# Performance work log

Hardware: AMD Instinct MI355X
Metric: run time of the kernel (lower is better)

Reference implementation:

```python
import jax, jax.numpy as jnp
import numpy as np

B, D, C, W, H = 2, 8, 256, 84, 84
NUM_HEADS = 8
WS = (2, 7, 7)
SS = (1, 3, 3)
MLP_RATIO = 4
EPS = 1e-5


def _rel_pos_index(ws):
    # static int index table (N, N), matches WindowAttention3D buffer
    coords = np.stack(np.meshgrid(np.arange(ws[0]), np.arange(ws[1]), np.arange(ws[2]), indexing='ij'))
    cf = coords.reshape(3, -1)
    rel = (cf[:, :, None] - cf[:, None, :]).transpose(1, 2, 0).copy()
    rel[:, :, 0] += ws[0] - 1
    rel[:, :, 1] += ws[1] - 1
    rel[:, :, 2] += ws[2] - 1
    rel[:, :, 0] *= (2 * ws[1] - 1) * (2 * ws[2] - 1)
    rel[:, :, 1] *= 2 * ws[2] - 1
    return rel.sum(-1)


def _attn_mask(Dp, Hp, Wp, ws, ss):
    # static additive shift mask (nW, N, N), matches create_mask
    m = np.zeros((Dp, Hp, Wp))
    cnt = 0
    for d in (slice(0, -ws[0]), slice(-ws[0], -ss[0]), slice(-ss[0], None)):
        for h in (slice(0, -ws[1]), slice(-ws[1], -ss[1]), slice(-ss[1], None)):
            for w in (slice(0, -ws[2]), slice(-ws[2], -ss[2]), slice(-ss[2], None)):
                m[d, h, w] = cnt
                cnt += 1
    mw = m.reshape(Dp // ws[0], ws[0], Hp // ws[1], ws[1], Wp // ws[2], ws[2])
    mw = mw.transpose(0, 2, 4, 1, 3, 5).reshape(-1, ws[0] * ws[1] * ws[2])
    diff = mw[:, None, :] - mw[:, :, None]
    return np.where(diff != 0, -100.0, 0.0).astype(np.float32)


def _layernorm(x, g, b):
    mu = x.mean(-1, keepdims=True)
    var = ((x - mu) ** 2).mean(-1, keepdims=True)
    return (x - mu) * jax.lax.rsqrt(var + EPS) * g + b


def setup_inputs():
    key = jax.random.key(0)
    ks = jax.random.split(key, 6)
    hidden = C * MLP_RATIO
    nbias = (2 * WS[0] - 1) * (2 * WS[1] - 1) * (2 * WS[2] - 1)
    s = lambda k, shape, sc=0.02: jax.random.normal(k, shape, jnp.float32) * sc
    return dict(
        x=jax.random.normal(ks[0], (B, D, C, W, H), jnp.float32),
        norm1_g=jnp.ones((C,), jnp.float32), norm1_b=jnp.zeros((C,), jnp.float32),
        qkv_w=s(ks[1], (3 * C, C)),
        rpb_table=s(ks[2], (nbias, NUM_HEADS)),
        proj_w=s(ks[3], (C, C)), proj_b=jnp.zeros((C,), jnp.float32),
        norm2_g=jnp.ones((C,), jnp.float32), norm2_b=jnp.zeros((C,), jnp.float32),
        fc1_w=s(ks[4], (hidden, C)), fc1_b=jnp.zeros((hidden,), jnp.float32),
        fc2_w=s(ks[5], (C, hidden)), fc2_b=jnp.zeros((C,), jnp.float32),
    )


def reference(x, norm1_g, norm1_b, qkv_w, rpb_table, proj_w, proj_b,
              norm2_g, norm2_b, fc1_w, fc1_b, fc2_w, fc2_b):
    # x: (B, D, C, W, H) -> (B, D, H, W, C)
    xp = jnp.transpose(x, (0, 1, 4, 3, 2))
    Bn, Dn, Hn, Wn, Cn = xp.shape
    wd, wh, ww = WS
    N = wd * wh * ww
    nW = (Dn // wd) * (Hn // wh) * (Wn // ww)
    head_dim = Cn // NUM_HEADS
    scale = head_dim ** -0.5

    rel_idx = _rel_pos_index(WS)                      # (N, N) static
    mask = jnp.asarray(_attn_mask(Dn, Hn, Wn, WS, SS))  # (nW, N, N) static

    shortcut = xp
    h1 = _layernorm(xp, norm1_g, norm1_b)
    # cyclic shift (D,H,W divisible by window -> no padding)
    h1 = jnp.roll(h1, shift=(-SS[0], -SS[1], -SS[2]), axis=(1, 2, 3))
    # window partition -> (B*nW, N, C)
    xw = h1.reshape(Bn, Dn // wd, wd, Hn // wh, wh, Wn // ww, ww, Cn)
    xw = jnp.transpose(xw, (0, 1, 3, 5, 2, 4, 6, 7)).reshape(-1, N, Cn)
    B_ = xw.shape[0]

    qkv = (xw @ qkv_w.T).reshape(B_, N, 3, NUM_HEADS, head_dim)
    qkv = jnp.transpose(qkv, (2, 0, 3, 1, 4))  # (3, B_, h, N, hd)
    q, k, v = qkv[0] * scale, qkv[1], qkv[2]
    attn = jnp.einsum('bhnd,bhmd->bhnm', q, k)
    bias = rpb_table[rel_idx.reshape(-1)].reshape(N, N, NUM_HEADS)
    attn = attn + jnp.transpose(bias, (2, 0, 1))[None]
    attn = attn.reshape(Bn, nW, NUM_HEADS, N, N) + mask[None, :, None]
    attn = jax.nn.softmax(attn.reshape(B_, NUM_HEADS, N, N), axis=-1)
    out = jnp.einsum('bhnm,bhmd->bhnd', attn, v)
    out = jnp.transpose(out, (0, 2, 1, 3)).reshape(B_, N, Cn)
    out = out @ proj_w.T + proj_b

    # window reverse -> (B, D, H, W, C)
    out = out.reshape(Bn, Dn // wd, Hn // wh, Wn // ww, wd, wh, ww, Cn)
    out = jnp.transpose(out, (0, 1, 4, 2, 5, 3, 6, 7)).reshape(Bn, Dn, Hn, Wn, Cn)
    out = jnp.roll(out, shift=(SS[0], SS[1], SS[2]), axis=(1, 2, 3))

    xres = shortcut + out
    # MLP block (torch GELU = exact erf)
    h2 = _layernorm(xres, norm2_g, norm2_b)
    h2 = jax.nn.gelu(h2 @ fc1_w.T + fc1_b, approximate=False)
    h2 = h2 @ fc2_w.T + fc2_b
    y = xres + h2
    return jnp.transpose(y, (0, 1, 4, 3, 2))  # back to (B, D, C, W, H)
```

## Files before the change

kernel.cpp:

```cpp
#include <hip/hip_runtime.h>
#include <hip/hip_bf16.h>
#include <cstdint>
#include <cstddef>

#define B_   2
#define D_   8
#define C_   256
#define W_   84
#define H_   84
#define NH   8
#define HD   32
#define NTOK 98
#define WH   7056
#define M2   56448
#define NWC  576

typedef __attribute__((ext_vector_type(8))) short sh8;
typedef __attribute__((ext_vector_type(4))) float f32x4;
typedef __hip_bfloat16 bf16;

__global__ __launch_bounds__(256) void k_f2b(const float* __restrict__ in,
                                             bf16* __restrict__ out, int n) {
  int i = blockIdx.x * 256 + threadIdx.x;
  if (i < n) out[i] = __float2bfloat16(in[i]);
}

__global__ __launch_bounds__(256) void k_bias(const float* __restrict__ rpb,
                                              float* __restrict__ tbl) {
  int cls = blockIdx.x >> 3, h = blockIdx.x & 7;
  int dB = cls >> 2, hB = (cls >> 1) & 1, wB = cls & 1;
  for (int idx = threadIdx.x; idx < 112 * 112; idx += 256) {
    int r = idx / 112, c = idx - (idx / 112) * 112;
    int rt = r < 98 ? r : 97, ct = c < 98 ? c : 97;
    int jdr = rt / 49, remr = rt % 49, jhr = remr / 7, jwr = remr % 7;
    int jdc = ct / 49, remc = ct % 49, jhc = remc / 7, jwc = remc % 7;
    int bir = jdr * 169 + jhr * 13 + jwr, bic = jdc * 169 + jhc * 13 + jwc;
    int dgr = dB ? ((6 + jdr) < 7 ? 1 : 2) : 0;
    int hgr = hB ? ((77 + jhr) < 81 ? 1 : 2) : 0;
    int wgr = wB ? ((77 + jwr) < 81 ? 1 : 2) : 0;
    int dgc = dB ? ((6 + jdc) < 7 ? 1 : 2) : 0;
    int hgc = hB ? ((77 + jhc) < 81 ? 1 : 2) : 0;
    int wgc = wB ? ((77 + jwc) < 81 ? 1 : 2) : 0;
    int cir = dgr * 9 + hgr * 3 + wgr, cic = dgc * 9 + hgc * 3 + wgc;
    float v = rpb[(bir - bic + 253) * 8 + h] + (cir == cic ? 0.f : -100.f);
    tbl[((size_t)(cls * 8 + h) * 112 + r) * 112 + c] = v;
  }
}

__device__ __forceinline__ int inv_row(int b, int d0, int w0, int h0) {
  int sd = (d0 + 7) & 7;
  int lid = (sd >> 1) & 1, jd = sd & 1;
  int sh = h0 + 81; if (sh >= 84) sh -= 84;
  int sw = w0 + 81; if (sw >= 84) sw -= 84;
  int ih = sh / 7, jh = sh - ih * 7;
  int iw = sw / 7, jw = sw - iw * 7;
  return (b * 288 + lid * 144 + ih * 12 + iw) * 98 + jd * 49 + jh * 7 + jw;
}

__global__ __launch_bounds__(256) void k_xpose_w(const float* __restrict__ x,
                                                 float* __restrict__ xtw, int cchunk) {
  int blk = blockIdx.x;
  int ch = blk & 1;
  int t = blk >> 1;
  int w0 = t % 84;
  int t2 = t / 84;
  int i = t2 & 3, b = t2 >> 2;
  int d0 = (cchunk * 4 + 1 + i) & 7;
  __shared__ float tile[128][85];
  __shared__ int rtab[84];
  int tid = threadIdx.x;
  if (tid < 84) rtab[tid] = inv_row(b, d0, w0, tid);
  const float* src = x + ((size_t)(b * 8 + d0) * 256 + ch * 128) * WH + w0 * 84;
  for (int idx = tid; idx < 128 * 21; idx += 256) {
    int c = idx / 21, h4 = idx - c * 21;
    float4 v = *(const float4*)(src + (size_t)c * WH + h4 * 4);
    tile[c][h4 * 4 + 0] = v.x; tile[c][h4 * 4 + 1] = v.y;
    tile[c][h4 * 4 + 2] = v.z; tile[c][h4 * 4 + 3] = v.w;
  }
  __syncthreads();
  for (int idx = tid; idx < 84 * 128; idx += 256) {
    int h = idx >> 7, cc = idx & 127;
    xtw[(size_t)rtab[h] * 256 + ch * 128 + cc] = tile[cc][h];
  }
}

__global__ __launch_bounds__(256) void k_ln1_lin(
    const float* __restrict__ xtw, const float* __restrict__ g,
    const float* __restrict__ bb, bf16* __restrict__ xw) {
  int rl = blockIdx.x * 4 + (threadIdx.x >> 6);
  int lane = threadIdx.x & 63;
  int c0 = lane * 4;
  float4 v = *(const float4*)(xtw + (size_t)rl * 256 + c0);
  float s = v.x + v.y + v.z + v.w;
  float s2 = v.x * v.x + v.y * v.y + v.z * v.z + v.w * v.w;
#pragma unroll
  for (int off = 32; off; off >>= 1) { s += __shfl_xor(s, off, 64); s2 += __shfl_xor(s2, off, 64); }
  float mu = s * (1.f / 256.f);
  float var = s2 * (1.f / 256.f) - mu * mu;
  float rs = rsqrtf(var + 1e-5f);
  float4 gg = *(const float4*)(g + c0);
  float4 bv = *(const float4*)(bb + c0);
  bf16 tmp[4];
  tmp[0] = __float2bfloat16((v.x - mu) * rs * gg.x + bv.x);
  tmp[1] = __float2bfloat16((v.y - mu) * rs * gg.y + bv.y);
  tmp[2] = __float2bfloat16((v.z - mu) * rs * gg.z + bv.z);
  tmp[3] = __float2bfloat16((v.w - mu) * rs * gg.w + bv.w);
  *(ushort4*)(&xw[(size_t)rl * 256 + c0]) = *(ushort4*)tmp;
}

__device__ __forceinline__ float gelu_fast(float v) {
  float x = v * 0.70710678118f;
  float ax = fabsf(x);
  float t = 1.0f / (1.0f + 0.3275911f * ax);
  float y = t * (0.254829592f + t * (-0.284496736f +
            t * (1.421413741f + t * (-1.453152027f + t * 1.061405429f))));
  float er = 1.0f - y * __expf(-ax * ax);
  er = copysignf(er, x);
  return 0.5f * v * (1.0f + er);
}

template <int EPI>
__global__ __launch_bounds__(256) void k_gemm_bt(
    const bf16* __restrict__ A, const bf16* __restrict__ Bw,
    int M, int N, int K,
    const float* __restrict__ bias, const float* __restrict__ res,
    void* __restrict__ outv) {
  __shared__ __align__(16) short smem[24576];
  int nwg = gridDim.x;
  int orig = blockIdx.x;
  int q8 = nwg >> 3, r8 = nwg & 7;
  int xcd = orig & 7, lwg = orig >> 3;
  int bid = (xcd < r8 ? xcd * (q8 + 1) : r8 * (q8 + 1) + (xcd - r8) * q8) + lwg;
  int nbn = N >> 7;
  int bm = bid / nbn, bn = bid - bm * nbn;
  int tid = threadIdx.x;
  int lane = tid & 63, wv = tid >> 6;
  int wr = wv >> 1, wc = wv & 1;
  f32x4 acc[4][4] = {};
  const short* Ag = (const short*)A + (size_t)bm * 128 * K;
  const short* Bg = (const short*)Bw + (size_t)bn * 128 * K;
  int rIn = lane >> 2;
  int cSrc = ((lane & 3) ^ ((lane >> 3) & 3)) * 8;
  int nk = K >> 5;

  auto stage = [&](int buf, int kt) {
    short* sA = smem + buf * 8192;
    short* sB = sA + 4096;
#pragma unroll
    for (int rr = 0; rr < 2; ++rr) {
      int r0 = wv * 32 + rr * 16;
      const short* ga = Ag + (size_t)(r0 + rIn) * K + kt * 32 + cSrc;
      const short* gb = Bg + (size_t)(r0 + rIn) * K + kt * 32 + cSrc;
      __builtin_amdgcn_global_load_lds(
          (const __attribute__((address_space(1))) void*)ga,
          (__attribute__((address_space(3))) void*)&sA[r0 * 32], 16, 0, 0);
      __builtin_amdgcn_global_load_lds(
          (const __attribute__((address_space(1))) void*)gb,
          (__attribute__((address_space(3))) void*)&sB[r0 * 32], 16, 0, 0);
    }
  };

  stage(0, 0);
  stage(1, 1);
  int rdBuf = 0, wrBuf = 2;
  int rb = wr * 64 + (lane & 15);
  int cb = wc * 64 + (lane & 15);
  int kswz = (((lane >> 4) ^ ((lane >> 1) & 3))) * 8;
  for (int kt = 0; kt < nk; ++kt) {
    __builtin_amdgcn_s_barrier();
    if (kt + 2 < nk) {
      stage(wrBuf, kt + 2);
      asm volatile("s_waitcnt vmcnt(8)" ::: "memory");
    } else if (kt + 1 < nk) {
      asm volatile("s_waitcnt vmcnt(4)" ::: "memory");
    } else {
      asm volatile("s_waitcnt vmcnt(0)" ::: "memory");
    }
    __builtin_amdgcn_s_barrier();
    __builtin_amdgcn_sched_barrier(0);
    const short* sA = smem + rdBuf * 8192;
    const short* sB = sA + 4096;
    sh8 af[4], bfr[4];
#pragma unroll
    for (int m = 0; m < 4; ++m) af[m] = *(const sh8*)&sA[(rb + m * 16) * 32 + kswz];
#pragma unroll
    for (int n2 = 0; n2 < 4; ++n2) bfr[n2] = *(const sh8*)&sB[(cb + n2 * 16) * 32 + kswz];
#pragma unroll
    for (int m = 0; m < 4; ++m)
#pragma unroll
      for (int n2 = 0; n2 < 4; ++n2)
        acc[m][n2] = __builtin_amdgcn_mfma_f32_16x16x32_bf16(af[m], bfr[n2], acc[m][n2], 0, 0, 0);
    rdBuf = (rdBuf + 1 == 3) ? 0 : rdBuf + 1;
    wrBuf = (wrBuf + 1 == 3) ? 0 : wrBuf + 1;
  }
  int rbase = bm * 128 + wr * 64 + ((lane >> 4) << 2);
  int cbase = bn * 128 + wc * 64 + (lane & 15);
#pragma unroll
  for (int m = 0; m < 4; ++m) {
#pragma unroll
    for (int j = 0; j < 4; ++j) {
      int r = rbase + m * 16 + j;
#pragma unroll
      for (int n2 = 0; n2 < 4; ++n2) {
        int cc = cbase + n2 * 16;
        float v = acc[m][n2][j];
        if (EPI == 2) {
          v += bias[cc] + res[(size_t)r * N + cc];
          ((float*)outv)[(size_t)r * N + cc] = v;
        } else {
          if (bias) v += bias[cc];
          if (EPI == 1) v = gelu_fast(v);
          ((bf16*)outv)[(size_t)r * N + cc] = __float2bfloat16(v);
        }
      }
    }
  }
}

__global__ __launch_bounds__(64) void k_attn_mfma(
    const bf16* __restrict__ qkv, const float* __restrict__ tbl,
    bf16* __restrict__ aout, int idbase) {
  int blk = blockIdx.x;
  int wl = blk >> 3, h = blk & 7;
  int lid = (wl / 144) & 1;
  int id = idbase + lid;
  int rem = wl % 144;
  int ih = rem / 12, iw = rem - ih * 12;
  int cls = ((id == 3) ? 4 : 0) + ((ih == 11) ? 2 : 0) + ((iw == 11) ? 1 : 0);
  const float* bt = tbl + (size_t)(cls * 8 + h) * 112 * 112;
  int lane = threadIdx.x;
  __shared__ __align__(16) short vt[32][136];
  __shared__ __align__(16) short pb[16][136];
  sh8 z = {};
  for (int i = lane; i < 544; i += 64) *((sh8*)&vt[0][0] + i) = z;
  for (int i = lane; i < 272; i += 64) *((sh8*)&pb[0][0] + i) = z;
  __syncthreads();
  const size_t base = (size_t)wl * NTOK * 768;
  for (int i = lane; i < 98 * 8; i += 64) {
    int c = i >> 3, d4 = (i & 7) * 4;
    ushort4 vu = *(const ushort4*)&qkv[base + (size_t)c * 768 + 512 + h * 32 + d4];
    vt[d4 + 0][c] = (short)vu.x; vt[d4 + 1][c] = (short)vu.y;
    vt[d4 + 2][c] = (short)vu.z; vt[d4 + 3][c] = (short)vu.w;
  }
  int kq = (lane >> 4) * 8;
  sh8 kf[7];
#pragma unroll
  for (int jt = 0; jt < 7; ++jt) {
    int c = jt * 16 + (lane & 15);
    kf[jt] = *(const sh8*)&qkv[base + (size_t)c * 768 + 256 + h * 32 + kq];
  }
  __syncthreads();
  sh8 vb[2][4];
#pragma unroll
  for (int dt = 0; dt < 2; ++dt)
#pragma unroll
    for (int k2 = 0; k2 < 4; ++k2)
      vb[dt][k2] = *(const sh8*)&vt[dt * 16 + (lane & 15)][k2 * 32 + kq];

  const float scale = 0.17677669529663687f;
  f32x4 zc = {};
  int rband = (lane >> 4) * 4;
  for (int it = 0; it < 7; ++it) {
    int rq = it * 16 + (lane & 15);
    sh8 qf = *(const sh8*)&qkv[base + (size_t)rq * 768 + h * 32 + kq];
    f32x4 s[7];
#pragma unroll
    for (int jt = 0; jt < 7; ++jt)
      s[jt] = __builtin_amdgcn_mfma_f32_16x16x32_bf16(qf, kf[jt], zc, 0, 0, 0);
    float p[7][4], linv[4];
#pragma unroll
    for (int j = 0; j < 4; ++j) {
      int r2 = it * 16 + rband + j;
      float rs = 0.f;
#pragma unroll
      for (int jt = 0; jt < 7; ++jt) {
        int c = jt * 16 + (lane & 15);
        float v = s[jt][j] * scale + bt[r2 * 112 + c];
        float e = __expf(v);
        if (jt == 6 && (lane & 15) >= 2) e = 0.f;
        p[jt][j] = e;
        rs += e;
      }
      rs += __shfl_xor(rs, 1, 64); rs += __shfl_xor(rs, 2, 64);
      rs += __shfl_xor(rs, 4, 64); rs += __shfl_xor(rs, 8, 64);
      linv[j] = 1.f / rs;
    }
#pragma unroll
    for (int j = 0; j < 4; ++j)
#pragma unroll
      for (int jt = 0; jt < 7; ++jt) {
        bf16 bv = __float2bfloat16(p[jt][j] * linv[j]);
        pb[rband + j][jt * 16 + (lane & 15)] = *(short*)&bv;
      }
    __syncthreads();
    sh8 pa[4];
#pragma unroll
    for (int k2 = 0; k2 < 4; ++k2)
      pa[k2] = *(const sh8*)&pb[lane & 15][k2 * 32 + kq];
    f32x4 o[2] = {};
#pragma unroll
    for (int dt = 0; dt < 2; ++dt)
#pragma unroll
      for (int k2 = 0; k2 < 4; ++k2)
        o[dt] = __builtin_amdgcn_mfma_f32_16x16x32_bf16(pa[k2], vb[dt][k2], o[dt], 0, 0, 0);
#pragma unroll
    for (int j = 0; j < 4; ++j) {
      int r2 = it * 16 + rband + j;
      if (r2 < 98) {
#pragma unroll
        for (int dt = 0; dt < 2; ++dt) {
          bf16 ov = __float2bfloat16(o[dt][j]);
          aout[((size_t)wl * 98 + r2) * 256 + h * 32 + dt * 16 + (lane & 15)] = ov;
        }
      }
    }
    __syncthreads();
  }
}

__global__ __launch_bounds__(256) void k_xres_ln2_lin(
    const float* __restrict__ xtw, const bf16* __restrict__ pout,
    const float* __restrict__ g, const float* __restrict__ bb,
    float* __restrict__ xres, bf16* __restrict__ ln2) {
  int rl = blockIdx.x * 4 + (threadIdx.x >> 6);
  int lane = threadIdx.x & 63;
  int c0 = lane * 4;
  float4 v = *(const float4*)(xtw + (size_t)rl * 256 + c0);
  ushort4 pu = *(const ushort4*)(pout + (size_t)rl * 256 + c0);
  v.x += __bfloat162float(*(bf16*)&pu.x);
  v.y += __bfloat162float(*(bf16*)&pu.y);
  v.z += __bfloat162float(*(bf16*)&pu.z);
  v.w += __bfloat162float(*(bf16*)&pu.w);
  *(float4*)(xres + (size_t)rl * 256 + c0) = v;
  float s = v.x + v.y + v.z + v.w;
  float s2 = v.x * v.x + v.y * v.y + v.z * v.z + v.w * v.w;
#pragma unroll
  for (int off = 32; off; off >>= 1) { s += __shfl_xor(s, off, 64); s2 += __shfl_xor(s2, off, 64); }
  float mu = s * (1.f / 256.f);
  float var = s2 * (1.f / 256.f) - mu * mu;
  float rs = rsqrtf(var + 1e-5f);
  float4 gg = *(const float4*)(g + c0);
  float4 bv = *(const float4*)(bb + c0);
  bf16 tmp[4];
  tmp[0] = __float2bfloat16((v.x - mu) * rs * gg.x + bv.x);
  tmp[1] = __float2bfloat16((v.y - mu) * rs * gg.y + bv.y);
  tmp[2] = __float2bfloat16((v.z - mu) * rs * gg.z + bv.z);
  tmp[3] = __float2bfloat16((v.w - mu) * rs * gg.w + bv.w);
  *(ushort4*)(&ln2[(size_t)rl * 256 + c0]) = *(ushort4*)tmp;
}

__global__ __launch_bounds__(256) void k_final_c(const float* __restrict__ y,
                                                 float* __restrict__ out, int cchunk) {
  int t = blockIdx.x;
  int w0 = t % 84;
  int t2 = t / 84;
  int i = t2 & 3, b = t2 >> 2;
  int d0 = (cchunk * 4 + 1 + i) & 7;
  __shared__ float tile[84][65];
  __shared__ int rtab[84];
  int tid = threadIdx.x;
  if (tid < 84) rtab[tid] = inv_row(b, d0, w0, tid);
  __syncthreads();
  for (int c0 = 0; c0 < 256; c0 += 64) {
    for (int idx = tid; idx < 84 * 64; idx += 256) {
      int hh = idx >> 6, cc = idx & 63;
      tile[hh][cc] = y[(size_t)rtab[hh] * 256 + c0 + cc];
    }
    __syncthreads();
    for (int idx = tid; idx < 64 * 84; idx += 256) {
      int cc = idx / 84, hh = idx - cc * 84;
      out[((((size_t)b * 8 + d0) * 256 + c0 + cc) * 84 + w0) * 84 + hh] = tile[hh][cc];
    }
    __syncthreads();
  }
}

extern "C" void kernel_launch(void* const* d_in, const int* in_sizes, int n_in,
                              void* d_out, int out_size, void* d_ws, size_t ws_size,
                              hipStream_t stream) {
  const float* x      = (const float*)d_in[0];
  const float* n1g    = (const float*)d_in[1];
  const float* n1b    = (const float*)d_in[2];
  const float* qkv_w  = (const float*)d_in[3];
  const float* rpb    = (const float*)d_in[4];
  const float* proj_w = (const float*)d_in[5];
  const float* proj_b = (const float*)d_in[6];
  const float* n2g    = (const float*)d_in[7];
  const float* n2b    = (const float*)d_in[8];
  const float* fc1_w  = (const float*)d_in[9];
  const float* fc1_b  = (const float*)d_in[10];
  const float* fc2_w  = (const float*)d_in[11];
  const float* fc2_b  = (const float*)d_in[12];
  float* out = (float*)d_out;

  char* w = (char*)d_ws;
  size_t off = 0;
  bf16* wq = (bf16*)(w + off); off += (size_t)768 * 256 * 2;
  bf16* wp = (bf16*)(w + off); off += (size_t)256 * 256 * 2;
  bf16* w1 = (bf16*)(w + off); off += (size_t)1024 * 256 * 2;
  bf16* w2 = (bf16*)(w + off); off += (size_t)1024 * 256 * 2;
  float* tbl = (float*)(w + off); off += (size_t)8 * 8 * 112 * 112 * 4;

  float* xtw  = (float*)(w + off); off += (size_t)M2 * 1024;
  bf16*  xw   = (bf16*)(w + off);  off += (size_t)M2 * 512;
  char*  qreg = w + off;           off += (size_t)M2 * 1536;
  float* xres = (float*)(w + off); off += (size_t)M2 * 1024;
  bf16*  hid  = (bf16*)(w + off);
  bf16* qkvb = (bf16*)qreg;
  bf16* aout = xw;
  bf16* pout = (bf16*)qreg;
  bf16* ln2b = (bf16*)(qreg + (size_t)M2 * 512);
  float* ybuf = xtw;

  int subTiles = 21;
  if (off + (size_t)441 * 128 * 2048 + 1024 <= ws_size) subTiles = 441;
  else if (off + (size_t)147 * 128 * 2048 + 1024 <= ws_size) subTiles = 147;
  else if (off + (size_t)49 * 128 * 2048 + 1024 <= ws_size) subTiles = 49;
  const int nsub = 441 / subTiles;
  const int MSUB = subTiles * 128;

  k_f2b<<<(196608 + 255) / 256, 256, 0, stream>>>(qkv_w, wq, 196608);
  k_f2b<<<(65536 + 255) / 256, 256, 0, stream>>>(proj_w, wp, 65536);
  k_f2b<<<(262144 + 255) / 256, 256, 0, stream>>>(fc1_w, w1, 262144);
  k_f2b<<<(262144 + 255) / 256, 256, 0, stream>>>(fc2_w, w2, 262144);
  k_bias<<<64, 256, 0, stream>>>(rpb, tbl);

  for (int c = 0; c < 2; ++c) {
    k_xpose_w<<<1344, 256, 0, stream>>>(x, xtw, c);
    k_ln1_lin<<<M2 / 4, 256, 0, stream>>>(xtw, n1g, n1b, xw);
    k_gemm_bt<0><<<441 * 6, 256, 0, stream>>>(xw, wq, M2, 768, 256, nullptr, nullptr, qkvb);
    k_attn_mfma<<<NWC * NH, 64, 0, stream>>>(qkvb, tbl, aout, 2 * c);
    k_gemm_bt<0><<<441 * 2, 256, 0, stream>>>(aout, wp, M2, 256, 256, proj_b, nullptr, pout);
    k_xres_ln2_lin<<<M2 / 4, 256, 0, stream>>>(xtw, pout, n2g, n2b, xres, ln2b);
    for (int s = 0; s < nsub; ++s) {
      size_t m0 = (size_t)s * MSUB;
      k_gemm_bt<1><<<subTiles * 8, 256, 0, stream>>>(
          ln2b + m0 * 256, w1, MSUB, 1024, 256, fc1_b, nullptr, hid);
      k_gemm_bt<2><<<subTiles * 2, 256, 0, stream>>>(
          hid, w2, MSUB, 256, 1024, fc2_b, xres + m0 * 256, ybuf + m0 * 256);
    }
    k_final_c<<<672, 256, 0, stream>>>(ybuf, out, c);
  }
}
```

Measured before the change: 789.7 us.

## Switch GEMM to double-buffered LDS with compile-time K and higher occupancy

The GEMM kernel now takes K as a template parameter so the k-loop can be fully unrolled with precomputed global and LDS pointers. LDS staging drops from three buffers to two, which cuts shared memory per block, and launch bounds request 5 waves per SIMD. MFMA sections are wrapped in s_setprio to favour compute issue. The cost is a shallower prefetch depth, so load latency may be hidden less well within each block, traded against more resident blocks per CU.

```diff
diff --git a/kernel.cpp b/kernel.cpp
--- a/kernel.cpp
+++ b/kernel.cpp
@@ -18,6 +18,9 @@
 typedef __attribute__((ext_vector_type(8))) short sh8;
 typedef __attribute__((ext_vector_type(4))) float f32x4;
 typedef __hip_bfloat16 bf16;
+
+#define AS1 __attribute__((address_space(1)))
+#define AS3 __attribute__((address_space(3)))
 
 __global__ __launch_bounds__(256) void k_f2b(const float* __restrict__ in,
                                              bf16* __restrict__ out, int n) {
@@ -119,13 +122,14 @@
   return 0.5f * v * (1.0f + er);
 }
 
-template <int EPI>
-__global__ __launch_bounds__(256) void k_gemm_bt(
+template <int EPI, int NK>
+__global__ __launch_bounds__(256, 5) void k_gemm_bt(
     const bf16* __restrict__ A, const bf16* __restrict__ Bw,
-    int M, int N, int K,
+    int M, int N,
     const float* __restrict__ bias, const float* __restrict__ res,
     void* __restrict__ outv) {
-  __shared__ __align__(16) short smem[24576];
+  constexpr int K = NK * 32;
+  __shared__ __align__(16) short smem[16384];
   int nwg = gridDim.x;
   int orig = blockIdx.x;
   int q8 = nwg >> 3, r8 = nwg & 7;
@@ -141,57 +145,54 @@
   const short* Bg = (const short*)Bw + (size_t)bn * 128 * K;
   int rIn = lane >> 2;
   int cSrc = ((lane & 3) ^ ((lane >> 3) & 3)) * 8;
-  int nk = K >> 5;
-
-  auto stage = [&](int buf, int kt) {
-    short* sA = smem + buf * 8192;
-    short* sB = sA + 4096;
-#pragma unroll
-    for (int rr = 0; rr < 2; ++rr) {
-      int r0 = wv * 32 + rr * 16;
-      const short* ga = Ag + (size_t)(r0 + rIn) * K + kt * 32 + cSrc;
-      const short* gb = Bg + (size_t)(r0 + rIn) * K + kt * 32 + cSrc;
-      __builtin_amdgcn_global_load_lds(
-          (const __attribute__((address_space(1))) void*)ga,
-          (__attribute__((address_space(3))) void*)&sA[r0 * 32], 16, 0, 0);
-      __builtin_amdgcn_global_load_lds(
-          (const __attribute__((address_space(1))) void*)gb,
-          (__attribute__((address_space(3))) void*)&sB[r0 * 32], 16, 0, 0);
-    }
-  };
-
-  stage(0, 0);
-  stage(1, 1);
-  int rdBuf = 0, wrBuf = 2;
+  const short* gA0 = Ag + (size_t)(wv * 32 + rIn) * K + cSrc;
+  const short* gA1 = gA0 + 16 * K;
+  const short* gB0 = Bg + (size_t)(wv * 32 + rIn) * K + cSrc;
+  const short* gB1 = gB0 + 16 * K;
+  const int ldsW = wv * 1024;
   int rb = wr * 64 + (lane & 15);
   int cb = wc * 64 + (lane & 15);
-  int kswz = (((lane >> 4) ^ ((lane >> 1) & 3))) * 8;
-  for (int kt = 0; kt < nk; ++kt) {
+  int kswz = ((lane >> 4) ^ ((lane >> 1) & 3)) * 8;
+  const short* rdA = smem + rb * 32 + kswz;
+  const short* rdB = smem + 4096 + cb * 32 + kswz;
+
+  __builtin_amdgcn_global_load_lds((const AS1 void*)gA0, (AS3 void*)&smem[ldsW], 16, 0, 0);
+  __builtin_amdgcn_global_load_lds((const AS1 void*)gA1, (AS3 void*)&smem[ldsW + 512], 16, 0, 0);
+  __builtin_amdgcn_global_load_lds((const AS1 void*)gB0, (AS3 void*)&smem[4096 + ldsW], 16, 0, 0);
+  __builtin_amdgcn_global_load_lds((const AS1 void*)gB1, (AS3 void*)&smem[4096 + ldsW + 512], 16, 0, 0);
+
+#pragma unroll
+  for (int kt = 0; kt < NK; ++kt) {
+    const int buf = kt & 1;
     __builtin_amdgcn_s_barrier();
-    if (kt + 2 < nk) {
-      stage(wrBuf, kt + 2);
-      asm volatile("s_waitcnt vmcnt(8)" ::: "memory");
-    } else if (kt + 1 < nk) {
+    if (kt + 1 < NK) {
+      const int wb = (buf ^ 1) * 8192;
+      __builtin_amdgcn_global_load_lds((const AS1 void*)(gA0 + (kt + 1) * 32),
+                                       (AS3 void*)&smem[wb + ldsW], 16, 0, 0);
+      __builtin_amdgcn_global_load_lds((const AS1 void*)(gA1 + (kt + 1) * 32),
+                                       (AS3 void*)&smem[wb + ldsW + 512], 16, 0, 0);
+      __builtin_amdgcn_global_load_lds((const AS1 void*)(gB0 + (kt + 1) * 32),
+                                       (AS3 void*)&smem[wb + 4096 + ldsW], 16, 0, 0);
+      __builtin_amdgcn_global_load_lds((const AS1 void*)(gB1 + (kt + 1) * 32),
+                                       (AS3 void*)&smem[wb + 4096 + ldsW + 512], 16, 0, 0);
       asm volatile("s_waitcnt vmcnt(4)" ::: "memory");
     } else {
       asm volatile("s_waitcnt vmcnt(0)" ::: "memory");
     }
     __builtin_amdgcn_s_barrier();
     __builtin_amdgcn_sched_barrier(0);
-    const short* sA = smem + rdBuf * 8192;
-    const short* sB = sA + 4096;
     sh8 af[4], bfr[4];
 #pragma unroll
-    for (int m = 0; m < 4; ++m) af[m] = *(const sh8*)&sA[(rb + m * 16) * 32 + kswz];
-#pragma unroll
-    for (int n2 = 0; n2 < 4; ++n2) bfr[n2] = *(const sh8*)&sB[(cb + n2 * 16) * 32 + kswz];
+    for (int m = 0; m < 4; ++m) af[m] = *(const sh8*)(rdA + buf * 8192 + m * 512);
+#pragma unroll
+    for (int n2 = 0; n2 < 4; ++n2) bfr[n2] = *(const sh8*)(rdB + buf * 8192 + n2 * 512);
+    __builtin_amdgcn_s_setprio(1);
 #pragma unroll
     for (int m = 0; m < 4; ++m)
 #pragma unroll
       for (int n2 = 0; n2 < 4; ++n2)
         acc[m][n2] = __builtin_amdgcn_mfma_f32_16x16x32_bf16(af[m], bfr[n2], acc[m][n2], 0, 0, 0);
-    rdBuf = (rdBuf + 1 == 3) ? 0 : rdBuf + 1;
-    wrBuf = (wrBuf + 1 == 3) ? 0 : wrBuf + 1;
+    __builtin_amdgcn_s_setprio(0);
   }
   int rbase = bm * 128 + wr * 64 + ((lane >> 4) << 2);
   int cbase = bn * 128 + wc * 64 + (lane & 15);
@@ -428,16 +429,16 @@
   for (int c = 0; c < 2; ++c) {
     k_xpose_w<<<1344, 256, 0, stream>>>(x, xtw, c);
     k_ln1_lin<<<M2 / 4, 256, 0, stream>>>(xtw, n1g, n1b, xw);
-    k_gemm_bt<0><<<441 * 6, 256, 0, stream>>>(xw, wq, M2, 768, 256, nullptr, nullptr, qkvb);
+    k_gemm_bt<0, 8><<<441 * 6, 256, 0, stream>>>(xw, wq, M2, 768, nullptr, nullptr, qkvb);
     k_attn_mfma<<<NWC * NH, 64, 0, stream>>>(qkvb, tbl, aout, 2 * c);
-    k_gemm_bt<0><<<441 * 2, 256, 0, stream>>>(aout, wp, M2, 256, 256, proj_b, nullptr, pout);
+    k_gemm_bt<0, 8><<<441 * 2, 256, 0, stream>>>(aout, wp, M2, 256, proj_b, nullptr, pout);
     k_xres_ln2_lin<<<M2 / 4, 256, 0, stream>>>(xtw, pout, n2g, n2b, xres, ln2b);
     for (int s = 0; s < nsub; ++s) {
       size_t m0 = (size_t)s * MSUB;
-      k_gemm_bt<1><<<subTiles * 8, 256, 0, stream>>>(
-          ln2b + m0 * 256, w1, MSUB, 1024, 256, fc1_b, nullptr, hid);
-      k_gemm_bt<2><<<subTiles * 2, 256, 0, stream>>>(
-          hid, w2, MSUB, 256, 1024, fc2_b, xres + m0 * 256, ybuf + m0 * 256);
+      k_gemm_bt<1, 8><<<subTiles * 8, 256, 0, stream>>>(
+          ln2b + m0 * 256, w1, MSUB, 1024, fc1_b, nullptr, hid);
+      k_gemm_bt<2, 32><<<subTiles * 2, 256, 0, stream>>>(
+          hid, w2, MSUB, 256, fc2_b, xres + m0 * 256, ybuf + m0 * 256);
     }
     k_final_c<<<672, 256, 0, stream>>>(ybuf, out, c);
   }
```

Result: slower. 1.348 ms (+70.8%).
